# Kernel tuning notes

Hardware: AMD Instinct MI355X
Metric: run time of the kernel (lower is better)

The kernel has to match this reference:

```python
import jax, jax.numpy as jnp
import numpy as np

D, H, HK, DH = 2048, 32, 8, 64
RQ = RKV = 48
RO = RFF = 1024
INTER = 8192
B, T = 2, 1024
THETA = 10000.0
EPS = 1e-5
NEG = -1e30


def _rms(x, w):
    v = jnp.mean(x * x, axis=-1, keepdims=True)
    return x * jax.lax.rsqrt(v + EPS) * w


def _proj_per_head(x, Us, V):
    # x:[B,T,D], V:[h,r,D], Us:[h,dh,r] -> [B,h,T,dh]
    xr = jnp.einsum('btd,hrd->bthr', x, V)
    return jnp.einsum('bthr,hdr->bhtd', xr, Us)


def _rope_cos_sin(position_ids, dh):
    inv = 1.0 / (THETA ** (jnp.arange(0, dh, 2, dtype=jnp.float32) / dh))
    ang = position_ids.astype(jnp.float32)[:, None] * inv[None, :]   # [T, dh/2]
    ang = jnp.repeat(ang, 2, axis=-1)                                # interleaved, per source
    return jnp.cos(ang), jnp.sin(ang)                                # [T, dh]


def _rotate_half(x):
    d = x.shape[-1] // 2
    return jnp.concatenate([-x[..., d:], x[..., :d]], axis=-1)


def setup_inputs() -> dict:
    key = jax.random.key(0)
    ks = jax.random.split(key, 18)
    g = lambda i, shape, s: (jax.random.normal(ks[i], shape, jnp.float32) * s)
    return {
        'x': g(0, (B, T, D), 1.0),
        'position_ids': jnp.arange(T, dtype=jnp.int32),
        'ln1_w': jnp.ones((D,), jnp.float32),
        'ln2_w': jnp.ones((D,), jnp.float32),
        'q_Us': g(1, (H, DH, RQ), 0.05), 'q_V': g(2, (H, RQ, D), 0.05),
        'k_Us': g(3, (HK, DH, RKV), 0.05), 'k_V': g(4, (HK, RKV, D), 0.05),
        'v_Us': g(5, (HK, DH, RKV), 0.05), 'v_V': g(6, (HK, RKV, D), 0.05),
        'o_Us': g(7, (D, RO), 0.02), 'o_V': g(8, (RO, H * DH), 0.02),
        'g_Us': g(9, (INTER, RFF), 0.02), 'g_V': g(10, (RFF, D), 0.02),
        'u_Us': g(11, (INTER, RFF), 0.02), 'u_V': g(12, (RFF, D), 0.02),
        'd_Us': g(13, (D, RFF), 0.02), 'd_V': g(14, (RFF, INTER), 0.02),
    }


def reference(x, position_ids, ln1_w, ln2_w,
              q_Us, q_V, k_Us, k_V, v_Us, v_V,
              o_Us, o_V, g_Us, g_V, u_Us, u_V, d_Us, d_V):
    Bx, Tx, Dx = x.shape
    n_rep = H // HK

    # ---- attention sub-block ----
    h = _rms(x, ln1_w)
    q = _proj_per_head(h, q_Us, q_V)          # [B,H,T,dh]
    k = _proj_per_head(h, k_Us, k_V)          # [B,Hk,T,dh]
    v = _proj_per_head(h, v_Us, v_V)          # [B,Hk,T,dh]

    cos, sin = _rope_cos_sin(position_ids, DH)          # [T,dh]
    cos = cos[None, None]; sin = sin[None, None]
    q = q * cos + _rotate_half(q) * sin
    k = k * cos + _rotate_half(k) * sin

    k = jnp.repeat(k, n_rep, axis=1)          # GQA expand -> [B,H,T,dh]
    v = jnp.repeat(v, n_rep, axis=1)

    scale = 1.0 / jnp.sqrt(jnp.float32(DH))
    scores = jnp.einsum('bhtd,bhsd->bhts', q, k) * scale
    causal = jnp.tril(jnp.ones((Tx, Tx), bool))
    scores = jnp.where(causal[None, None], scores, NEG)
    p = jax.nn.softmax(scores, axis=-1)
    attn = jnp.einsum('bhts,bhsd->bhtd', p, v)            # [B,H,T,dh]
    attn = attn.transpose(0, 2, 1, 3).reshape(Bx, Tx, H * DH)

    # low-rank o projection: W_o ~= o_Us @ o_V
    ar = jnp.einsum('btk,rk->btr', attn, o_V)
    attn_out = jnp.einsum('btr,dr->btd', ar, o_Us)
    x = x + attn_out

    # ---- low-rank SwiGLU MLP ----
    h2 = _rms(x, ln2_w)
    gate = jnp.einsum('btr,ir->bti', jnp.einsum('btd,rd->btr', h2, g_V), g_Us)
    up = jnp.einsum('btr,ir->bti', jnp.einsum('btd,rd->btr', h2, u_V), u_Us)
    inner = jax.nn.silu(gate) * up
    down = jnp.einsum('btr,dr->btd', jnp.einsum('bti,ri->btr', inner, d_V), d_Us)
    return x + down
```

## Files before the change

### kernel.cpp

```cpp
#include <hip/hip_runtime.h>

typedef unsigned short u16;
typedef unsigned int u32;
typedef unsigned long long u64;

typedef __bf16 bf16x8 __attribute__((ext_vector_type(8)));
typedef float f32x4 __attribute__((ext_vector_type(4)));

__device__ __forceinline__ float bf2f(u16 u) {
  union { u32 i; float f; } v; v.i = ((u32)u) << 16; return v.f;
}
__device__ __forceinline__ u16 f2bf(float f) {
  union { float f; u32 i; } v; v.f = f;
  u32 r = v.i + 0x7fff + ((v.i >> 16) & 1);
  return (u16)(r >> 16);
}
__device__ __forceinline__ u32 packbf(float a, float b) {
  return (u32)f2bf(a) | ((u32)f2bf(b) << 16);
}

__device__ __forceinline__ void gload_lds16(const u16* g, u16* l) {
  __builtin_amdgcn_global_load_lds(
      (const __attribute__((address_space(1))) void*)g,
      (__attribute__((address_space(3))) void*)l, 16, 0, 0);
}

struct CvtTab {
  const void* src[16];
  u64 doff[16];
  u32 bstart[16];
};

__global__ __launch_bounds__(256)
void convert_k(CvtTab tab, u16* __restrict__ wbase, const u32* __restrict__ w2,
               u32* __restrict__ flag_out)
{
  const u32 f = (w2[0] == 0x3F803F80u) ? 0u : 1u;
  if (blockIdx.x == 0 && threadIdx.x == 0) *flag_out = f;
  const int blk = blockIdx.x;
  int t = 15;
#pragma unroll
  for (int i = 15; i >= 1; i--) if (blk < (int)tab.bstart[i]) t = i - 1;
  const u64 eoff = (u64)(blk - tab.bstart[t]) * 2048 + threadIdx.x * 8;
  u16* dst = wbase + tab.doff[t] + eoff;
  if (f == 0) {
    uint4 v = *(const uint4*)((const u16*)tab.src[t] + eoff);
    *(uint4*)dst = v;
  } else {
    const float* s = (const float*)tab.src[t] + eoff;
    uint4 lo = *(const uint4*)s;
    uint4 hi = *(const uint4*)(s + 4);
    union { u32 i; float fv; } c0,c1,c2,c3,c4,c5,c6,c7;
    c0.i = lo.x; c1.i = lo.y; c2.i = lo.z; c3.i = lo.w;
    c4.i = hi.x; c5.i = hi.y; c6.i = hi.z; c7.i = hi.w;
    uint4 pb;
    pb.x = packbf(c0.fv, c1.fv); pb.y = packbf(c2.fv, c3.fv);
    pb.z = packbf(c4.fv, c5.fv); pb.w = packbf(c6.fv, c7.fv);
    *(uint4*)dst = pb;
  }
}

template<int EPI, int TM, int TN, int BK>
__global__ __launch_bounds__(256)
void gemm_bt(const u16* __restrict__ A, const u16* __restrict__ B,
             void* Cout, const void* R,
             int K, int lda, int ldc, int pstride, const u32* __restrict__ dflag)
{
  constexpr int NFM = TM / 32;
  constexpr int NFN = TN / 32;
  constexpr int CH = BK / 8;
  constexpr int ISA = TM * CH / 256;
  constexpr int ISB = TN * CH / 256;
  __shared__ u16 sA[TM * BK];
  __shared__ u16 sB[TN * BK];
  const u32 f = *dflag;
  const int tid  = threadIdx.x;
  const int bm   = blockIdx.y * TM;
  const int bn   = blockIdx.x * TN;
  const int Klen = K / gridDim.z;
  const int kbase = blockIdx.z * Klen;
  const int wave = tid >> 6, lane = tid & 63;
  const int wm = (wave >> 1) * (TM / 2), wn = (wave & 1) * (TN / 2);
  const int lr = lane & 15, lq = lane >> 4;

  f32x4 acc[NFM][NFN];
#pragma unroll
  for (int i = 0; i < NFM; i++)
#pragma unroll
    for (int j = 0; j < NFN; j++) { f32x4 z = {0.f,0.f,0.f,0.f}; acc[i][j] = z; }

  int sAoff[ISA], sArow[ISA];
#pragma unroll
  for (int j = 0; j < ISA; j++) {
    int s = (wave * ISA + j) * 64 + lane;
    sArow[j] = s / CH;
    sAoff[j] = ((s % CH) ^ (sArow[j] & 7)) * 8;
  }
  int sBoff[ISB], sBrow[ISB];
#pragma unroll
  for (int j = 0; j < ISB; j++) {
    int s = (wave * ISB + j) * 64 + lane;
    sBrow[j] = s / CH;
    sBoff[j] = ((s % CH) ^ (sBrow[j] & 7)) * 8;
  }

  for (int k0 = kbase; k0 < kbase + Klen; k0 += BK) {
#pragma unroll
    for (int j = 0; j < ISA; j++)
      gload_lds16(A + (size_t)(bm + sArow[j]) * lda + k0 + sAoff[j],
                  &sA[(wave * ISA + j) * 512]);
#pragma unroll
    for (int j = 0; j < ISB; j++)
      gload_lds16(B + (size_t)(bn + sBrow[j]) * K + k0 + sBoff[j],
                  &sB[(wave * ISB + j) * 512]);
    __syncthreads();
#pragma unroll
    for (int kk = 0; kk < BK; kk += 32) {
      bf16x8 af[NFM], bfr[NFN];
#pragma unroll
      for (int i = 0; i < NFM; i++)
        af[i] = *(const bf16x8*)
            &sA[(wm + i * 16 + lr) * BK + ((((kk >> 3) + lq) ^ (lr & 7)) * 8)];
#pragma unroll
      for (int i = 0; i < NFN; i++)
        bfr[i] = *(const bf16x8*)
            &sB[(wn + i * 16 + lr) * BK + ((((kk >> 3) + lq) ^ (lr & 7)) * 8)];
#pragma unroll
      for (int i = 0; i < NFM; i++)
#pragma unroll
        for (int j = 0; j < NFN; j++)
          acc[i][j] = __builtin_amdgcn_mfma_f32_16x16x32_bf16(af[i], bfr[j], acc[i][j], 0, 0, 0);
    }
    __syncthreads();
  }

  u16* outz = (u16*)Cout + (size_t)blockIdx.z * pstride;
#pragma unroll
  for (int i = 0; i < NFM; i++) {
#pragma unroll
    for (int j = 0; j < NFN; j++) {
#pragma unroll
      for (int e = 0; e < 4; e++) {
        int row = bm + wm + i * 16 + lq * 4 + e;
        int col = bn + wn + j * 16 + lr;
        size_t idx = (size_t)row * ldc + col;
        float v = acc[i][j][e];
        if (EPI == 0) {
          outz[idx] = f2bf(v);
        } else if (EPI == 1) {
          float rv = f ? ((const float*)R)[idx] : bf2f(((const u16*)R)[idx]);
          ((float*)Cout)[idx] = v + rv;
        } else if (EPI == 2) {
          float s = v + ((const float*)R)[idx];
          if (f) ((float*)Cout)[idx] = s;
          else   ((u16*)Cout)[idx] = f2bf(s);
        }
      }
    }
  }
}

__global__ __launch_bounds__(256)
void gemm_gu(const u16* __restrict__ A, const u16* __restrict__ Bg,
             const u16* __restrict__ Bu, u16* __restrict__ Cout,
             int K, int lda, int ldc)
{
  constexpr int TILE = 128, BK = 64, NF = 4, CH = 8, ITER_S = 4;
  __shared__ u16 sA[TILE * BK];
  __shared__ u16 sB[TILE * BK];
  const int tid  = threadIdx.x;
  const int bm   = blockIdx.y * TILE;
  const int bn   = blockIdx.x * TILE;
  const int wave = tid >> 6, lane = tid & 63;
  const int wm = (wave >> 1) * 64, wn = (wave & 1) * 64;
  const int lr = lane & 15, lq = lane >> 4;

  f32x4 accG[NF][NF], accU[NF][NF];
#pragma unroll
  for (int i = 0; i < NF; i++)
#pragma unroll
    for (int j = 0; j < NF; j++) {
      f32x4 z = {0.f,0.f,0.f,0.f}; accG[i][j] = z; accU[i][j] = z;
    }

  int scA[ITER_S], scRow[ITER_S];
#pragma unroll
  for (int j = 0; j < ITER_S; j++) {
    int s = (wave * ITER_S + j) * 64 + lane;
    scRow[j] = s / CH;
    scA[j] = ((s % CH) ^ (scRow[j] & 7)) * 8;
  }

#pragma unroll
  for (int ph = 0; ph < 2; ph++) {
    const u16* Ap = A + (ph ? 1024 : 0);
    const u16* Bp = ph ? Bu : Bg;
    for (int k0 = 0; k0 < K; k0 += BK) {
#pragma unroll
      for (int j = 0; j < ITER_S; j++) {
        gload_lds16(Ap + (size_t)(bm + scRow[j]) * lda + k0 + scA[j],
                    &sA[(wave * ITER_S + j) * 512]);
        gload_lds16(Bp + (size_t)(bn + scRow[j]) * K + k0 + scA[j],
                    &sB[(wave * ITER_S + j) * 512]);
      }
      __syncthreads();
#pragma unroll
      for (int kk = 0; kk < BK; kk += 32) {
        bf16x8 af[NF], bfr[NF];
#pragma unroll
        for (int i = 0; i < NF; i++)
          af[i] = *(const bf16x8*)
              &sA[(wm + i * 16 + lr) * BK + ((((kk >> 3) + lq) ^ (lr & 7)) * 8)];
#pragma unroll
        for (int i = 0; i < NF; i++)
          bfr[i] = *(const bf16x8*)
              &sB[(wn + i * 16 + lr) * BK + ((((kk >> 3) + lq) ^ (lr & 7)) * 8)];
        if (ph == 0) {
#pragma unroll
          for (int i = 0; i < NF; i++)
#pragma unroll
            for (int j = 0; j < NF; j++)
              accG[i][j] = __builtin_amdgcn_mfma_f32_16x16x32_bf16(af[i], bfr[j], accG[i][j], 0, 0, 0);
        } else {
#pragma unroll
          for (int i = 0; i < NF; i++)
#pragma unroll
            for (int j = 0; j < NF; j++)
              accU[i][j] = __builtin_amdgcn_mfma_f32_16x16x32_bf16(af[i], bfr[j], accU[i][j], 0, 0, 0);
        }
      }
      __syncthreads();
    }
  }

#pragma unroll
  for (int i = 0; i < NF; i++) {
#pragma unroll
    for (int j = 0; j < NF; j++) {
#pragma unroll
      for (int e = 0; e < 4; e++) {
        int row = bm + wm + i * 16 + lq * 4 + e;
        int col = bn + wn + j * 16 + lr;
        float g = accG[i][j][e];
        float inner = g / (1.f + __expf(-g)) * accU[i][j][e];
        Cout[(size_t)row * ldc + col] = f2bf(inner);
      }
    }
  }
}

__global__ __launch_bounds__(256)
void reduce2_k(const u16* __restrict__ p, u16* __restrict__ out, int nel)
{
  size_t i = ((size_t)blockIdx.x * 256 + threadIdx.x) * 8;
  uint4 a = *(const uint4*)(p + i);
  uint4 b = *(const uint4*)(p + (size_t)nel + i);
  u32 aa[4] = {a.x, a.y, a.z, a.w};
  u32 bb[4] = {b.x, b.y, b.z, b.w};
  u32 rr[4];
#pragma unroll
  for (int k = 0; k < 4; k++) {
    float s0 = bf2f((u16)aa[k]) + bf2f((u16)bb[k]);
    float s1 = bf2f((u16)(aa[k] >> 16)) + bf2f((u16)(bb[k] >> 16));
    rr[k] = packbf(s0, s1);
  }
  uint4 o; o.x = rr[0]; o.y = rr[1]; o.z = rr[2]; o.w = rr[3];
  *(uint4*)(out + i) = o;
}

template<int XSRC>
__global__ __launch_bounds__(256)
void rmsnorm_k(const void* __restrict__ xin, const u16* __restrict__ w,
               u16* __restrict__ out, const u32* __restrict__ dflag)
{
  const u32 f = *dflag;
  const int n = blockIdx.x, tid = threadIdx.x;
  const size_t base = (size_t)n * 2048 + tid * 8;
  float v[8]; float ss = 0.f;
  if (XSRC == 1 || f) {
    const float* xp = (const float*)xin + base;
    float4 lo = *(const float4*)xp;
    float4 hi = *(const float4*)(xp + 4);
    v[0]=lo.x; v[1]=lo.y; v[2]=lo.z; v[3]=lo.w;
    v[4]=hi.x; v[5]=hi.y; v[6]=hi.z; v[7]=hi.w;
  } else {
    uint4 xv = *(const uint4*)((const u16*)xin + base);
    const u32 xw[4] = {xv.x, xv.y, xv.z, xv.w};
#pragma unroll
    for (int q = 0; q < 4; q++) {
      v[2*q]   = bf2f((u16)xw[q]);
      v[2*q+1] = bf2f((u16)(xw[q] >> 16));
    }
  }
#pragma unroll
  for (int i = 0; i < 8; i++) ss += v[i] * v[i];
#pragma unroll
  for (int o = 32; o >= 1; o >>= 1) ss += __shfl_xor(ss, o, 64);
  __shared__ float red[4];
  if ((tid & 63) == 0) red[tid >> 6] = ss;
  __syncthreads();
  float tot = red[0] + red[1] + red[2] + red[3];
  float rms = rsqrtf(tot * (1.f / 2048.f) + 1e-5f);
  uint4 wv = *(const uint4*)(w + tid * 8);
  const u32 ww[4] = {wv.x, wv.y, wv.z, wv.w};
  u32 rr[4];
#pragma unroll
  for (int q = 0; q < 4; q++) {
    float o0 = v[2*q]   * rms * bf2f((u16)ww[q]);
    float o1 = v[2*q+1] * rms * bf2f((u16)(ww[q] >> 16));
    rr[q] = packbf(o0, o1);
  }
  uint4 o; o.x = rr[0]; o.y = rr[1]; o.z = rr[2]; o.w = rr[3];
  *(uint4*)(out + base) = o;
}

template<int ROPE, int TRANS>
__global__ __launch_bounds__(256)
void qkv2_k(const u16* __restrict__ xr, const u16* __restrict__ Us,
            const int* __restrict__ pos, u16* __restrict__ out, int NH, int XS)
{
  const int h = blockIdx.y;
  const int tid = threadIdx.x;
  const int n = blockIdx.x * 8 + (tid >> 5);
  const int j = tid & 31;
  const u16* xrow = xr + (size_t)n * XS + h * 48;
  const u16* U = Us + (size_t)h * 64 * 48;
  const u16* Uj  = U + j * 48;
  const u16* Uj2 = U + (j + 32) * 48;
  float a = 0.f, b = 0.f;
#pragma unroll
  for (int c = 0; c < 6; c++) {
    uint4 xv4 = *(const uint4*)(xrow + c * 8);
    uint4 ua4 = *(const uint4*)(Uj + c * 8);
    uint4 ub4 = *(const uint4*)(Uj2 + c * 8);
    const u32 xw[4] = {xv4.x, xv4.y, xv4.z, xv4.w};
    const u32 aw[4] = {ua4.x, ua4.y, ua4.z, ua4.w};
    const u32 bw[4] = {ub4.x, ub4.y, ub4.z, ub4.w};
#pragma unroll
    for (int q = 0; q < 4; q++) {
      float x0 = bf2f((u16)xw[q]), x1 = bf2f((u16)(xw[q] >> 16));
      a += x0 * bf2f((u16)aw[q]) + x1 * bf2f((u16)(aw[q] >> 16));
      b += x0 * bf2f((u16)bw[q]) + x1 * bf2f((u16)(bw[q] >> 16));
    }
  }
  const int t = n & 1023, bb = n >> 10;
  float olo, ohi;
  if (ROPE) {
    float p = (float)pos[t];
    float inv_lo = powf(10000.f, -(float)(2 * (j >> 1)) * (1.f / 64.f));
    float inv_hi = powf(10000.f, -(float)(2 * (16 + (j >> 1))) * (1.f / 64.f));
    float sl, cl, sh, ch;
    sincosf(p * inv_lo, &sl, &cl);
    sincosf(p * inv_hi, &sh, &ch);
    olo = a * cl - b * sl;
    ohi = b * ch + a * sh;
  } else { olo = a; ohi = b; }
  if (TRANS == 0) {
    size_t ob = ((size_t)(bb * NH + h) * 1024 + t) * 64;
    out[ob + j] = f2bf(olo);
    out[ob + j + 32] = f2bf(ohi);
  } else {
    size_t ob = (size_t)(bb * NH + h) * 64 * 1024;
    out[ob + (size_t)j * 1024 + t] = f2bf(olo);
    out[ob + (size_t)(j + 32) * 1024 + t] = f2bf(ohi);
  }
}

__global__ __launch_bounds__(256)
void flash_k(const u16* __restrict__ Q, const u16* __restrict__ K,
             const u16* __restrict__ VT, u16* __restrict__ O)
{
  __shared__ u16 sQ[64 * 72];
  __shared__ u16 sK[128 * 72];
  __shared__ u16 sVT[64 * 136];
  __shared__ u16 sP[64 * 136];
  const int bh = blockIdx.x;
  const int b = bh >> 5, h = bh & 31, hk = h >> 2;
  const int t0 = (int)(gridDim.y - 1 - blockIdx.y) << 6;
  const int tid = threadIdx.x, wave = tid >> 6, lane = tid & 63;
  const int lr = lane & 15, lq = lane >> 4;
  const int qr = wave * 16;
  const size_t bhk = (size_t)(b * 8 + hk);
  const u16* Qb = Q + ((size_t)bh * 1024 + t0) * 64;
  const u16* Kb = K + bhk * 1024 * 64;
  const u16* Vb = VT + bhk * 64 * 1024;

#pragma unroll
  for (int i = 0; i < 2; i++) {
    int c = tid + i * 256;
    int row = c >> 3, col = (c & 7) * 8;
    *(uint4*)&sQ[row * 72 + col] = *(const uint4*)(Qb + row * 64 + col);
  }

  f32x4 acc[4];
#pragma unroll
  for (int dt = 0; dt < 4; dt++) { f32x4 z = {0.f,0.f,0.f,0.f}; acc[dt] = z; }
  float m[4], l[4];
#pragma unroll
  for (int e = 0; e < 4; e++) { m[e] = -3.0e38f; l[e] = 0.f; }

  const int ntiles = (t0 >> 7) + 1;
  for (int st = 0; st < ntiles; st++) {
    __syncthreads();
#pragma unroll
    for (int i = 0; i < 4; i++) {
      int c = tid + i * 256;
      int row = c >> 3, col = (c & 7) * 8;
      *(uint4*)&sK[row * 72 + col] =
          *(const uint4*)(Kb + (size_t)(st * 128 + row) * 64 + col);
    }
#pragma unroll
    for (int i = 0; i < 4; i++) {
      int c = tid + i * 256;
      int d = c >> 4, t8 = (c & 15) * 8;
      *(uint4*)&sVT[d * 136 + t8] =
          *(const uint4*)(Vb + (size_t)d * 1024 + st * 128 + t8);
    }
    __syncthreads();

    bf16x8 aq0 = *(const bf16x8*)&sQ[(qr + lr) * 72 + lq * 8];
    bf16x8 aq1 = *(const bf16x8*)&sQ[(qr + lr) * 72 + 32 + lq * 8];
    f32x4 sf[8];
#pragma unroll
    for (int nt = 0; nt < 8; nt++) {
      f32x4 z = {0.f,0.f,0.f,0.f};
      bf16x8 bk0 = *(const bf16x8*)&sK[(nt * 16 + lr) * 72 + lq * 8];
      bf16x8 bk1 = *(const bf16x8*)&sK[(nt * 16 + lr) * 72 + 32 + lq * 8];
      z = __builtin_amdgcn_mfma_f32_16x16x32_bf16(aq0, bk0, z, 0, 0, 0);
      z = __builtin_amdgcn_mfma_f32_16x16x32_bf16(aq1, bk1, z, 0, 0, 0);
      sf[nt] = z;
    }

    const int colbase = st * 128;
#pragma unroll
    for (int e = 0; e < 4; e++) {
      const int row = t0 + qr + lq * 4 + e;
      float tm = -3.0e38f;
#pragma unroll
      for (int nt = 0; nt < 8; nt++) {
        float v = sf[nt][e] * 0.125f;
        if (colbase + nt * 16 + lr > row) v = -1e30f;
        sf[nt][e] = v;
        tm = fmaxf(tm, v);
      }
      tm = fmaxf(tm, __shfl_xor(tm, 1, 64));
      tm = fmaxf(tm, __shfl_xor(tm, 2, 64));
      tm = fmaxf(tm, __shfl_xor(tm, 4, 64));
      tm = fmaxf(tm, __shfl_xor(tm, 8, 64));
      float mnew = fmaxf(m[e], tm);
      float alpha = __expf(m[e] - mnew);
      m[e] = mnew;
      float ts = 0.f;
#pragma unroll
      for (int nt = 0; nt < 8; nt++) {
        float p = __expf(sf[nt][e] - mnew);
        sP[(qr + lq * 4 + e) * 136 + nt * 16 + lr] = f2bf(p);
        ts += p;
      }
      ts += __shfl_xor(ts, 1, 64);
      ts += __shfl_xor(ts, 2, 64);
      ts += __shfl_xor(ts, 4, 64);
      ts += __shfl_xor(ts, 8, 64);
      l[e] = l[e] * alpha + ts;
#pragma unroll
      for (int dt = 0; dt < 4; dt++) acc[dt][e] *= alpha;
    }

#pragma unroll
    for (int kk = 0; kk < 4; kk++) {
      bf16x8 pa = *(const bf16x8*)&sP[(qr + lr) * 136 + kk * 32 + lq * 8];
#pragma unroll
      for (int dt = 0; dt < 4; dt++) {
        bf16x8 bv = *(const bf16x8*)&sVT[(dt * 16 + lr) * 136 + kk * 32 + lq * 8];
        acc[dt] = __builtin_amdgcn_mfma_f32_16x16x32_bf16(pa, bv, acc[dt], 0, 0, 0);
      }
    }
  }

#pragma unroll
  for (int e = 0; e < 4; e++) {
    float inv = 1.f / l[e];
    int t = t0 + qr + lq * 4 + e;
#pragma unroll
    for (int dt = 0; dt < 4; dt++) {
      size_t idx = ((size_t)(b * 1024 + t)) * 2048 + h * 64 + dt * 16 + lr;
      O[idx] = f2bf(acc[dt][e] * inv);
    }
  }
}

extern "C" void kernel_launch(void* const* d_in, const int* in_sizes, int n_in,
                              void* d_out, int out_size, void* d_ws, size_t ws_size,
                              hipStream_t stream)
{
  const void* x    = d_in[0];
  const int* pos   = (const int*)d_in[1];

  char* ws = (char*)d_ws;
  const size_t MB = 1048576;
  float* x1     = (float*)(ws + 0 * MB);
  u16*   gate   = (u16*)  (ws + 16 * MB);
  u16*   h1     = (u16*)  (ws + 16 * MB);
  u16*   attn   = (u16*)  (ws + 16 * MB);
  u16*   xr_all = (u16*)  (ws + 24 * MB);
  u16*   ar     = (u16*)  (ws + 24 * MB);
  u16*   h2     = (u16*)  (ws + 28 * MB);
  u16*   qb     = (u16*)  (ws + 33 * MB);
  u16*   kb     = (u16*)  (ws + 41 * MB);
  u16*   vbt    = (u16*)  (ws + 43 * MB);
  u16*   part   = (u16*)  (ws + 48 * MB);
  u16*   gr_ur  = (u16*)  (ws + 48 * MB);
  u16*   dr     = (u16*)  (ws + 56 * MB);
  u16*   wb     = (u16*)  (ws + 60 * MB);
  u32*   flag   = (u32*)  (ws + 60 * MB + 81043456);

  u16* wQKV = wb + 0;
  u16* wGU  = wb + 4718592;
  u16* oVc  = wb + 8912896;
  u16* oUsc = wb + 11010048;
  u16* gUsc = wb + 13107200;
  u16* uUsc = wb + 21495808;
  u16* dVc  = wb + 29884416;
  u16* dUsc = wb + 38273024;
  u16* qUsc = wb + 40370176;
  u16* kUsc = wb + 40468480;
  u16* vUsc = wb + 40493056;
  u16* ln1c = wb + 40517632;
  u16* ln2c = wb + 40519680;

  CvtTab tab;
  const int srcidx[16] = {5, 7, 9, 13, 15, 11, 10, 12, 14, 17, 16, 4, 6, 8, 2, 3};
  const u64 doff[16] = {0, 3145728, 3932160, 4718592, 6815744, 8912896, 11010048,
                        13107200, 21495808, 29884416, 38273024, 40370176,
                        40468480, 40493056, 40517632, 40519680};
  const u32 bstart[16] = {0, 1536, 1920, 2304, 3328, 4352, 5376, 6400, 10496,
                          14592, 18688, 19712, 19760, 19772, 19784, 19785};
  for (int i = 0; i < 16; i++) {
    tab.src[i] = d_in[srcidx[i]];
    tab.doff[i] = doff[i];
    tab.bstart[i] = bstart[i];
  }

  dim3 blk(256);
  const int PS = 2097152;

  convert_k<<<19786, blk, 0, stream>>>(tab, wb, (const u32*)d_in[2], flag);

  rmsnorm_k<0><<<2048, blk, 0, stream>>>(x, ln1c, h1, flag);

  gemm_bt<0,128,64,64><<<dim3(36, 16), blk, 0, stream>>>(h1, wQKV, xr_all, nullptr,
                                                         2048, 2048, 2304, 0, flag);

  qkv2_k<1,0><<<dim3(256, 32), blk, 0, stream>>>(xr_all,        qUsc, pos, qb, 32, 2304);
  qkv2_k<1,0><<<dim3(256, 8),  blk, 0, stream>>>(xr_all + 1536, kUsc, pos, kb, 8,  2304);
  qkv2_k<0,1><<<dim3(256, 8),  blk, 0, stream>>>(xr_all + 1920, vUsc, pos, vbt, 8, 2304);

  flash_k<<<dim3(64, 16), blk, 0, stream>>>(qb, kb, vbt, attn);

  gemm_bt<0,128,64,64><<<dim3(16, 16, 2), blk, 0, stream>>>(attn, oVc, part, nullptr,
                                                            2048, 2048, 1024, PS, flag);
  reduce2_k<<<1024, blk, 0, stream>>>(part, ar, PS);
  gemm_bt<1,128,64,64><<<dim3(32, 16), blk, 0, stream>>>(ar, oUsc, x1, x,
                                                         1024, 1024, 2048, 0, flag);

  rmsnorm_k<1><<<2048, blk, 0, stream>>>(x1, ln2c, h2, flag);

  gemm_bt<0,128,64,64><<<dim3(32, 16), blk, 0, stream>>>(h2, wGU, gr_ur, nullptr,
                                                         2048, 2048, 2048, 0, flag);

  gemm_gu<<<dim3(64, 16), blk, 0, stream>>>(gr_ur, gUsc, uUsc, gate,
                                            1024, 2048, 8192);

  gemm_bt<0,128,64,64><<<dim3(16, 16, 2), blk, 0, stream>>>(gate, dVc, part, nullptr,
                                                            8192, 8192, 1024, PS, flag);
  reduce2_k<<<1024, blk, 0, stream>>>(part, dr, PS);
  gemm_bt<2,128,64,64><<<dim3(32, 16), blk, 0, stream>>>(dr, dUsc, d_out, x1,
                                                         1024, 1024, 2048, 0, flag);
}
```

Before: 595.3 us.

## Split-K QKV and o_V GEMMs, fuse per-head q/k/v up-projections into one launch

```diff
diff --git a/kernel.cpp b/kernel.cpp
--- a/kernel.cpp
+++ b/kernel.cpp
@@ -268,6 +268,31 @@
   *(uint4*)(out + i) = o;
 }
 
+__global__ __launch_bounds__(256)
+void reduce4_k(const u16* __restrict__ p, u16* __restrict__ out, int nel)
+{
+  size_t i = ((size_t)blockIdx.x * 256 + threadIdx.x) * 8;
+  uint4 a = *(const uint4*)(p + i);
+  uint4 b = *(const uint4*)(p + (size_t)nel + i);
+  uint4 c = *(const uint4*)(p + 2 * (size_t)nel + i);
+  uint4 d = *(const uint4*)(p + 3 * (size_t)nel + i);
+  u32 aa[4] = {a.x, a.y, a.z, a.w};
+  u32 bb[4] = {b.x, b.y, b.z, b.w};
+  u32 cc[4] = {c.x, c.y, c.z, c.w};
+  u32 dd[4] = {d.x, d.y, d.z, d.w};
+  u32 rr[4];
+#pragma unroll
+  for (int k = 0; k < 4; k++) {
+    float s0 = (bf2f((u16)aa[k]) + bf2f((u16)bb[k])) +
+               (bf2f((u16)cc[k]) + bf2f((u16)dd[k]));
+    float s1 = (bf2f((u16)(aa[k] >> 16)) + bf2f((u16)(bb[k] >> 16))) +
+               (bf2f((u16)(cc[k] >> 16)) + bf2f((u16)(dd[k] >> 16)));
+    rr[k] = packbf(s0, s1);
+  }
+  uint4 o; o.x = rr[0]; o.y = rr[1]; o.z = rr[2]; o.w = rr[3];
+  *(uint4*)(out + i) = o;
+}
+
 template<int XSRC>
 __global__ __launch_bounds__(256)
 void rmsnorm_k(const void* __restrict__ xin, const u16* __restrict__ w,
@@ -314,17 +339,17 @@
   *(uint4*)(out + base) = o;
 }
 
-template<int ROPE, int TRANS>
-__global__ __launch_bounds__(256)
-void qkv2_k(const u16* __restrict__ xr, const u16* __restrict__ Us,
-            const int* __restrict__ pos, u16* __restrict__ out, int NH, int XS)
+__global__ __launch_bounds__(256)
+void qkv_all(const u16* __restrict__ xr, const u16* __restrict__ Us0,
+             const int* __restrict__ pos, u16* __restrict__ qb,
+             u16* __restrict__ kb, u16* __restrict__ vbt)
 {
   const int h = blockIdx.y;
   const int tid = threadIdx.x;
   const int n = blockIdx.x * 8 + (tid >> 5);
   const int j = tid & 31;
-  const u16* xrow = xr + (size_t)n * XS + h * 48;
-  const u16* U = Us + (size_t)h * 64 * 48;
+  const u16* xrow = xr + (size_t)n * 2304 + h * 48;
+  const u16* U = Us0 + (size_t)h * 3072;
   const u16* Uj  = U + j * 48;
   const u16* Uj2 = U + (j + 32) * 48;
   float a = 0.f, b = 0.f;
@@ -344,8 +369,8 @@
     }
   }
   const int t = n & 1023, bb = n >> 10;
-  float olo, ohi;
-  if (ROPE) {
+  float olo = a, ohi = b;
+  if (h < 40) {
     float p = (float)pos[t];
     float inv_lo = powf(10000.f, -(float)(2 * (j >> 1)) * (1.f / 64.f));
     float inv_hi = powf(10000.f, -(float)(2 * (16 + (j >> 1))) * (1.f / 64.f));
@@ -354,15 +379,19 @@
     sincosf(p * inv_hi, &sh, &ch);
     olo = a * cl - b * sl;
     ohi = b * ch + a * sh;
-  } else { olo = a; ohi = b; }
-  if (TRANS == 0) {
-    size_t ob = ((size_t)(bb * NH + h) * 1024 + t) * 64;
-    out[ob + j] = f2bf(olo);
-    out[ob + j + 32] = f2bf(ohi);
+  }
+  if (h < 32) {
+    size_t ob = ((size_t)(bb * 32 + h) * 1024 + t) * 64;
+    qb[ob + j] = f2bf(olo);
+    qb[ob + j + 32] = f2bf(ohi);
+  } else if (h < 40) {
+    size_t ob = ((size_t)(bb * 8 + (h - 32)) * 1024 + t) * 64;
+    kb[ob + j] = f2bf(olo);
+    kb[ob + j + 32] = f2bf(ohi);
   } else {
-    size_t ob = (size_t)(bb * NH + h) * 64 * 1024;
-    out[ob + (size_t)j * 1024 + t] = f2bf(olo);
-    out[ob + (size_t)(j + 32) * 1024 + t] = f2bf(ohi);
+    size_t ob = (size_t)(bb * 8 + (h - 40)) * 64 * 1024;
+    vbt[ob + (size_t)j * 1024 + t] = f2bf(olo);
+    vbt[ob + (size_t)(j + 32) * 1024 + t] = f2bf(ohi);
   }
 }
 
@@ -505,6 +534,7 @@
   u16*   xr_all = (u16*)  (ws + 24 * MB);
   u16*   ar     = (u16*)  (ws + 24 * MB);
   u16*   h2     = (u16*)  (ws + 28 * MB);
+  u16*   part28 = (u16*)  (ws + 28 * MB);
   u16*   qb     = (u16*)  (ws + 33 * MB);
   u16*   kb     = (u16*)  (ws + 41 * MB);
   u16*   vbt    = (u16*)  (ws + 43 * MB);
@@ -523,8 +553,6 @@
   u16* dVc  = wb + 29884416;
   u16* dUsc = wb + 38273024;
   u16* qUsc = wb + 40370176;
-  u16* kUsc = wb + 40468480;
-  u16* vUsc = wb + 40493056;
   u16* ln1c = wb + 40517632;
   u16* ln2c = wb + 40519680;
 
@@ -542,24 +570,24 @@
   }
 
   dim3 blk(256);
-  const int PS = 2097152;
+  const int PS  = 2097152;
+  const int PS2 = 4718592;
 
   convert_k<<<19786, blk, 0, stream>>>(tab, wb, (const u32*)d_in[2], flag);
 
   rmsnorm_k<0><<<2048, blk, 0, stream>>>(x, ln1c, h1, flag);
 
-  gemm_bt<0,128,64,64><<<dim3(36, 16), blk, 0, stream>>>(h1, wQKV, xr_all, nullptr,
-                                                         2048, 2048, 2304, 0, flag);
-
-  qkv2_k<1,0><<<dim3(256, 32), blk, 0, stream>>>(xr_all,        qUsc, pos, qb, 32, 2304);
-  qkv2_k<1,0><<<dim3(256, 8),  blk, 0, stream>>>(xr_all + 1536, kUsc, pos, kb, 8,  2304);
-  qkv2_k<0,1><<<dim3(256, 8),  blk, 0, stream>>>(xr_all + 1920, vUsc, pos, vbt, 8, 2304);
+  gemm_bt<0,128,64,64><<<dim3(36, 16, 2), blk, 0, stream>>>(h1, wQKV, part28, nullptr,
+                                                            2048, 2048, 2304, PS2, flag);
+  reduce2_k<<<2304, blk, 0, stream>>>(part28, xr_all, PS2);
+
+  qkv_all<<<dim3(256, 48), blk, 0, stream>>>(xr_all, qUsc, pos, qb, kb, vbt);
 
   flash_k<<<dim3(64, 16), blk, 0, stream>>>(qb, kb, vbt, attn);
 
-  gemm_bt<0,128,64,64><<<dim3(16, 16, 2), blk, 0, stream>>>(attn, oVc, part, nullptr,
+  gemm_bt<0,128,64,64><<<dim3(16, 16, 4), blk, 0, stream>>>(attn, oVc, part28, nullptr,
                                                             2048, 2048, 1024, PS, flag);
-  reduce2_k<<<1024, blk, 0, stream>>>(part, ar, PS);
+  reduce4_k<<<1024, blk, 0, stream>>>(part28, ar, PS);
   gemm_bt<1,128,64,64><<<dim3(32, 16), blk, 0, stream>>>(ar, oUsc, x1, x,
                                                          1024, 1024, 2048, 0, flag);
 
```

Result: no change. 592.2 us (-0.5%).
